# Performance work log

Measured on AMD Instinct MI355X. Metric: run time of the kernel, lower is better.

The kernel has to match this reference:

```python
import jax, jax.numpy as jnp
import numpy as np

K = 10          # number of clusters (static; matches randint fill_max)
ALPHA = 0.02    # intra-cluster margin
DELTA = 0.5     # inter-cluster margin
LAMBDA_INTRA = 1.0
LAMBDA_INTER = 1.0
MIN_WEIGHT = 50.0


def setup_inputs() -> dict:
    key = jax.random.key(0)
    k1, k2 = jax.random.split(key)
    x = jax.random.normal(k1, (8, 64, 240, 320), dtype=jnp.float32)
    # module assumes NORMALIZED unit vectors along channel dim
    x = x / jnp.maximum(jnp.linalg.norm(x, axis=1, keepdims=True), 1e-12)
    cluster_masks = jax.random.randint(k2, (8, 1, 240, 320), 0, K, dtype=jnp.int32)
    return {"x": x, "cluster_masks": cluster_masks}


def reference(x, cluster_masks):
    B, C, H, W = x.shape
    cm = cluster_masks[:, 0]  # (B, H, W) int
    # one-hot cluster assignment; out-of-range ids (e.g. -1 = unlabeled) -> all zeros
    onehot = jax.nn.one_hot(cm, K, dtype=x.dtype)  # (B, H, W, K)

    # ---- spherical cluster means (fused segment-reduce over H*W) ----
    sums = jnp.einsum('bchw,bhwk->bck', x, onehot)          # (B, C, K)
    counts = jnp.sum(onehot, axis=(1, 2))                    # (B, K)
    means = sums / (counts[:, None, :] + 1e-10)
    # F.normalize(p=2, dim=1): x / max(||x||, eps)
    means = means / jnp.maximum(jnp.linalg.norm(means, axis=1, keepdims=True), 1e-12)

    # ---- broadcast means back to pixels ----
    tiled = jnp.einsum('bck,bhwk->bchw', means, onehot)      # (B, C, H, W)

    labeled = (cm >= 0).astype(x.dtype)                      # (B, H, W)
    # cosine metric
    intra_d = labeled * (0.5 * (1.0 - jnp.sum(x * tiled, axis=1)))  # (B, H, W)

    # ---- per-cluster hard-example weighting ----
    indicator = (intra_d > ALPHA).astype(x.dtype)            # (B, H, W)
    N_k = jnp.einsum('bhw,bhwk->bk', indicator, onehot)      # (B, K)
    weights = jnp.einsum('bk,bhwk->bhw', N_k, onehot)        # (B, H, W)
    weights = jnp.maximum(weights, MIN_WEIGHT) * K
    intra_loss = jnp.sum(intra_d ** 2 / weights) / B
    intra_loss = LAMBDA_INTRA * jnp.where(jnp.sum(indicator) > 0, intra_loss, 0.0)

    # ---- inter-cluster hinge loss (K > 1 statically) ----
    inter_d = 0.5 * (1.0 - jnp.einsum('bck,bcl->bkl', means, means))  # (B, K, K)
    hinge = jnp.maximum(DELTA - inter_d, 0.0) * (1.0 - jnp.eye(K, dtype=x.dtype))
    inter_loss = LAMBDA_INTER * jnp.sum(hinge ** 2) / (K * (K - 1) / 2 * B)

    loss = intra_loss + inter_loss
    return (loss, intra_loss, inter_loss)
```

## Files before the change

kernel.cpp:

```cpp
#include <hip/hip_runtime.h>
#include <hip/hip_bf16.h>

#define B_ 8
#define C_ 64
#define H_ 240
#define W_ 320
#define HW_ (H_ * W_)
#define HW4_ (HW_ / 4)
#define K_ 10
#define ALPHA_ 0.02f
#define DELTA_ 0.5f
#define MIN_WEIGHT_ 50.0f


__global__ __launch_bounds__(256) void k1_sums(
    const float* __restrict__ x, const int* __restrict__ cm,
    float* __restrict__ sums, float* __restrict__ counts) {
  const int c = blockIdx.x;
  const int b = blockIdx.y;
  const int tid = threadIdx.x;

  const float4* __restrict__ xp =
      (const float4*)(x + (size_t)(b * C_ + c) * HW_);
  const int4* __restrict__ cp = (const int4*)(cm + (size_t)b * HW_);

  float acc[K_];
#pragma unroll
  for (int j = 0; j < K_; ++j) acc[j] = 0.f;
  float cnt[K_];
#pragma unroll
  for (int j = 0; j < K_; ++j) cnt[j] = 0.f;
  const bool do_cnt = (c == 0);

  for (int i = tid; i < HW4_; i += 256) {
    float4 v = xp[i];
    int4 k4 = cp[i];
#pragma unroll
    for (int j = 0; j < K_; ++j) {
      acc[j] += (k4.x == j ? v.x : 0.f);
      acc[j] += (k4.y == j ? v.y : 0.f);
      acc[j] += (k4.z == j ? v.z : 0.f);
      acc[j] += (k4.w == j ? v.w : 0.f);
    }
    if (do_cnt) {
#pragma unroll
      for (int j = 0; j < K_; ++j) {
        cnt[j] += (float)((k4.x == j) + (k4.y == j) + (k4.z == j) + (k4.w == j));
      }
    }
  }

#pragma unroll
  for (int j = 0; j < K_; ++j) {
    float v = acc[j];
    for (int off = 32; off > 0; off >>= 1) v += __shfl_down(v, off, 64);
    if ((tid & 63) == 0) atomicAdd(&sums[(b * C_ + c) * K_ + j], v);
  }
  if (do_cnt) {
#pragma unroll
    for (int j = 0; j < K_; ++j) {
      float v = cnt[j];
      for (int off = 32; off > 0; off >>= 1) v += __shfl_down(v, off, 64);
      if ((tid & 63) == 0) atomicAdd(&counts[b * K_ + j], v);
    }
  }
}

__global__ __launch_bounds__(256) void k2_means(
    const float* __restrict__ sums, const float* __restrict__ counts,
    float* __restrict__ means, float* __restrict__ interloss) {
  const int tid = threadIdx.x;

  if (tid < B_ * K_) {
    const int b = tid / K_;
    const int k = tid % K_;
    const float inv = 1.f / (counts[tid] + 1e-10f);
    float m[C_];
    float nrm2 = 0.f;
#pragma unroll
    for (int c = 0; c < C_; ++c) {
      float mm = sums[(b * C_ + c) * K_ + k] * inv;
      m[c] = mm;
      nrm2 += mm * mm;
    }
    const float rn = 1.f / fmaxf(sqrtf(nrm2), 1e-12f);
#pragma unroll
    for (int c = 0; c < C_; ++c) means[(b * C_ + c) * K_ + k] = m[c] * rn;
  }
  __syncthreads();

  float h2 = 0.f;
  for (int t = tid; t < B_ * 45; t += 256) {
    const int b = t / 45;
    int idx = t % 45;
    int k = 0, l = 0;
    for (k = 0; k < K_; ++k) {
      const int row = K_ - 1 - k;
      if (idx < row) { l = k + 1 + idx; break; }
      idx -= row;
    }
    float g = 0.f;
    for (int c = 0; c < C_; ++c)
      g += means[(b * C_ + c) * K_ + k] * means[(b * C_ + c) * K_ + l];
    const float inter_d = 0.5f * (1.f - g);
    const float h = fmaxf(DELTA_ - inter_d, 0.f);
    h2 += 2.f * h * h;
  }

  __shared__ float red[256];
  red[tid] = h2;
  __syncthreads();
  for (int s = 128; s > 0; s >>= 1) {
    if (tid < s) red[tid] += red[tid + s];
    __syncthreads();
  }
  if (tid == 0) interloss[0] = red[0] / (float)((K_ * (K_ - 1) / 2) * B_);
}

__global__ __launch_bounds__(256) void k3_intra(
    const float* __restrict__ x, const int* __restrict__ cm,
    const float* __restrict__ means, float* __restrict__ S2,
    float* __restrict__ Nk, float* __restrict__ indtot) {
  const int b = blockIdx.y;
  const int tid = threadIdx.x;

  __shared__ float mlds[C_ * K_];
  __shared__ float s2b[K_];
  __shared__ float nkb[K_];

  for (int i = tid; i < C_ * K_; i += 256) mlds[i] = means[b * C_ * K_ + i];
  if (tid < K_) { s2b[tid] = 0.f; nkb[tid] = 0.f; }
  __syncthreads();

  const int p4 = blockIdx.x * 256 + tid;
  const int4 k4 = ((const int4*)(cm + (size_t)b * HW_))[p4];
  const float4* __restrict__ xb = (const float4*)(x + (size_t)b * C_ * HW_);

  float d0 = 0.f, d1 = 0.f, d2 = 0.f, d3 = 0.f;
#pragma unroll 4
  for (int c = 0; c < C_; ++c) {
    float4 v = xb[c * HW4_ + p4];
    const float* mr = &mlds[c * K_];
    d0 += v.x * mr[k4.x];
    d1 += v.y * mr[k4.y];
    d2 += v.z * mr[k4.z];
    d3 += v.w * mr[k4.w];
  }

  const float i0 = 0.5f * (1.f - d0);
  const float i1 = 0.5f * (1.f - d1);
  const float i2 = 0.5f * (1.f - d2);
  const float i3 = 0.5f * (1.f - d3);

  atomicAdd(&s2b[k4.x], i0 * i0);
  atomicAdd(&s2b[k4.y], i1 * i1);
  atomicAdd(&s2b[k4.z], i2 * i2);
  atomicAdd(&s2b[k4.w], i3 * i3);
  atomicAdd(&nkb[k4.x], i0 > ALPHA_ ? 1.f : 0.f);
  atomicAdd(&nkb[k4.y], i1 > ALPHA_ ? 1.f : 0.f);
  atomicAdd(&nkb[k4.z], i2 > ALPHA_ ? 1.f : 0.f);
  atomicAdd(&nkb[k4.w], i3 > ALPHA_ ? 1.f : 0.f);
  __syncthreads();

  if (tid < K_) {
    atomicAdd(&S2[b * K_ + tid], s2b[tid]);
    atomicAdd(&Nk[b * K_ + tid], nkb[tid]);
    atomicAdd(indtot, nkb[tid]);
  }
}

__global__ void k4_final(const float* __restrict__ S2, const float* __restrict__ Nk,
                         const float* __restrict__ indtot,
                         const float* __restrict__ interloss,
                         float* __restrict__ out) {
  if (threadIdx.x == 0) {
    float intra = 0.f;
    for (int i = 0; i < B_ * K_; ++i) {
      const float w = fmaxf(Nk[i], MIN_WEIGHT_) * (float)K_;
      intra += S2[i] / w;
    }
    intra /= (float)B_;
    if (!(indtot[0] > 0.f)) intra = 0.f;
    const float inter = interloss[0];
    out[0] = intra + inter;
    out[1] = intra;
    out[2] = inter;
  }
}

extern "C" void kernel_launch(void* const* d_in, const int* in_sizes, int n_in,
                              void* d_out, int out_size, void* d_ws, size_t ws_size,
                              hipStream_t stream) {
  const float* x = (const float*)d_in[0];
  const int* cm = (const int*)d_in[1];

  float* ws = (float*)d_ws;
  float* sums = ws;
  float* counts = ws + 5120;
  float* means = ws + 5200;
  float* S2 = ws + 10320;
  float* Nk = ws + 10400;
  float* indtot = ws + 10480;
  float* interL = ws + 10481;

  hipMemsetAsync(d_ws, 0, 10482 * sizeof(float), stream);

  k1_sums<<<dim3(C_, B_), 256, 0, stream>>>(x, cm, sums, counts);
  k2_means<<<1, 256, 0, stream>>>(sums, counts, means, interL);
  k3_intra<<<dim3(HW4_ / 256, B_), 256, 0, stream>>>(x, cm, means, S2, Nk, indtot);
  k4_final<<<1, 64, 0, stream>>>(S2, Nk, indtot, interL, (float*)d_out);
}
```

Before: 297.8 us.

## Split k1 spatially across more blocks and split k3 channels across wavefronts

k1 gains a third grid dimension that splits each (channel, batch) pixel range into 8 chunks, taking the grid from 512 blocks to 4096 to fill the GPU better. The atomic merges into sums and counts grow eightfold. k3 now gives each 256-thread block 64 pixel-quads and has its four wavefronts each cover a quarter of the channels. Partial dot products are combined through shared memory before the per-cluster atomics. This adds more memory parallelism per pixel, at the cost of an extra shared-memory pass and barrier, four times as many blocks, and smaller contiguous reads per wavefront.

New measurement: 298.5 us. About the same (+0.3%).

```diff
diff --git a/kernel.cpp b/kernel.cpp
--- a/kernel.cpp
+++ b/kernel.cpp
@@ -12,13 +12,20 @@
 #define DELTA_ 0.5f
 #define MIN_WEIGHT_ 50.0f
 
+#define K1_SPLIT 8
+
 
 __global__ __launch_bounds__(256) void k1_sums(
     const float* __restrict__ x, const int* __restrict__ cm,
     float* __restrict__ sums, float* __restrict__ counts) {
   const int c = blockIdx.x;
   const int b = blockIdx.y;
+  const int z = blockIdx.z;
   const int tid = threadIdx.x;
+
+  const int chunk = HW4_ / K1_SPLIT;
+  const int lo = z * chunk;
+  const int hi = lo + chunk;
 
   const float4* __restrict__ xp =
       (const float4*)(x + (size_t)(b * C_ + c) * HW_);
@@ -32,7 +39,7 @@
   for (int j = 0; j < K_; ++j) cnt[j] = 0.f;
   const bool do_cnt = (c == 0);
 
-  for (int i = tid; i < HW4_; i += 256) {
+  for (int i = lo + tid; i < hi; i += 256) {
     float4 v = xp[i];
     int4 k4 = cp[i];
 #pragma unroll
@@ -123,8 +130,11 @@
     float* __restrict__ Nk, float* __restrict__ indtot) {
   const int b = blockIdx.y;
   const int tid = threadIdx.x;
+  const int lane_p = tid & 63;
+  const int grp = tid >> 6;
 
   __shared__ float mlds[C_ * K_];
+  __shared__ float4 pd[256];
   __shared__ float s2b[K_];
   __shared__ float nkb[K_];
 
@@ -132,13 +142,15 @@
   if (tid < K_) { s2b[tid] = 0.f; nkb[tid] = 0.f; }
   __syncthreads();
 
-  const int p4 = blockIdx.x * 256 + tid;
+  const int p4 = blockIdx.x * 64 + lane_p;
   const int4 k4 = ((const int4*)(cm + (size_t)b * HW_))[p4];
   const float4* __restrict__ xb = (const float4*)(x + (size_t)b * C_ * HW_);
 
   float d0 = 0.f, d1 = 0.f, d2 = 0.f, d3 = 0.f;
-#pragma unroll 4
-  for (int c = 0; c < C_; ++c) {
+  const int c0 = grp * (C_ / 4);
+#pragma unroll
+  for (int cc = 0; cc < C_ / 4; ++cc) {
+    const int c = c0 + cc;
     float4 v = xb[c * HW4_ + p4];
     const float* mr = &mlds[c * K_];
     d0 += v.x * mr[k4.x];
@@ -146,20 +158,28 @@
     d2 += v.z * mr[k4.z];
     d3 += v.w * mr[k4.w];
   }
-
-  const float i0 = 0.5f * (1.f - d0);
-  const float i1 = 0.5f * (1.f - d1);
-  const float i2 = 0.5f * (1.f - d2);
-  const float i3 = 0.5f * (1.f - d3);
-
-  atomicAdd(&s2b[k4.x], i0 * i0);
-  atomicAdd(&s2b[k4.y], i1 * i1);
-  atomicAdd(&s2b[k4.z], i2 * i2);
-  atomicAdd(&s2b[k4.w], i3 * i3);
-  atomicAdd(&nkb[k4.x], i0 > ALPHA_ ? 1.f : 0.f);
-  atomicAdd(&nkb[k4.y], i1 > ALPHA_ ? 1.f : 0.f);
-  atomicAdd(&nkb[k4.z], i2 > ALPHA_ ? 1.f : 0.f);
-  atomicAdd(&nkb[k4.w], i3 > ALPHA_ ? 1.f : 0.f);
+  pd[tid] = make_float4(d0, d1, d2, d3);
+  __syncthreads();
+
+  if (grp == 0) {
+    float4 a = pd[lane_p];
+    float4 bb = pd[lane_p + 64];
+    float4 cc = pd[lane_p + 128];
+    float4 dd = pd[lane_p + 192];
+    const float i0 = 0.5f * (1.f - (a.x + bb.x + cc.x + dd.x));
+    const float i1 = 0.5f * (1.f - (a.y + bb.y + cc.y + dd.y));
+    const float i2 = 0.5f * (1.f - (a.z + bb.z + cc.z + dd.z));
+    const float i3 = 0.5f * (1.f - (a.w + bb.w + cc.w + dd.w));
+
+    atomicAdd(&s2b[k4.x], i0 * i0);
+    atomicAdd(&s2b[k4.y], i1 * i1);
+    atomicAdd(&s2b[k4.z], i2 * i2);
+    atomicAdd(&s2b[k4.w], i3 * i3);
+    atomicAdd(&nkb[k4.x], i0 > ALPHA_ ? 1.f : 0.f);
+    atomicAdd(&nkb[k4.y], i1 > ALPHA_ ? 1.f : 0.f);
+    atomicAdd(&nkb[k4.z], i2 > ALPHA_ ? 1.f : 0.f);
+    atomicAdd(&nkb[k4.w], i3 > ALPHA_ ? 1.f : 0.f);
+  }
   __syncthreads();
 
   if (tid < K_) {
@@ -205,8 +225,8 @@
 
   hipMemsetAsync(d_ws, 0, 10482 * sizeof(float), stream);
 
-  k1_sums<<<dim3(C_, B_), 256, 0, stream>>>(x, cm, sums, counts);
+  k1_sums<<<dim3(C_, B_, K1_SPLIT), 256, 0, stream>>>(x, cm, sums, counts);
   k2_means<<<1, 256, 0, stream>>>(sums, counts, means, interL);
-  k3_intra<<<dim3(HW4_ / 256, B_), 256, 0, stream>>>(x, cm, means, S2, Nk, indtot);
+  k3_intra<<<dim3(HW4_ / 64, B_), 256, 0, stream>>>(x, cm, means, S2, Nk, indtot);
   k4_final<<<1, 64, 0, stream>>>(S2, Nk, indtot, interL, (float*)d_out);
 }
```
